# Performance work log

Hardware: AMD Instinct MI355X
Metric: run time of the kernel (lower is better)

Reference implementation:

```python
import jax, jax.numpy as jnp
import numpy as np
import math

B, S, D, H = 4, 2048, 1024, 16
HD = D // H  # head_size = 64


def setup_inputs() -> dict:
    key = jax.random.key(0)
    ks = jax.random.split(key, 12)
    s = 1.0 / math.sqrt(D)
    inp = {
        "query_in": jax.random.normal(ks[0], (B, S, D), jnp.float32),
        "key_in": jax.random.normal(ks[1], (B, S, D), jnp.float32),
        "values_in": jax.random.normal(ks[2], (B, S, D), jnp.float32),
        # causal mask, broadcast over batch and heads
        "mask": jnp.tril(jnp.ones((S, S), jnp.int32))[None, None],
        "Wq": jax.random.normal(ks[3], (D, D), jnp.float32) * s,
        "bq": jnp.zeros((D,), jnp.float32),
        "Wk": jax.random.normal(ks[4], (D, D), jnp.float32) * s,
        "bk": jnp.zeros((D,), jnp.float32),
        "Wv": jax.random.normal(ks[5], (D, D), jnp.float32) * s,
        "bv": jnp.zeros((D,), jnp.float32),
        "Wo": jax.random.normal(ks[6], (D, D), jnp.float32) * s,
        "bo": jnp.zeros((D,), jnp.float32),
    }
    return inp


def _heads(x):
    # [B,S,D] -> [B,H,S,HD]
    return x.reshape(B, S, H, HD).transpose(0, 2, 1, 3)


def reference(query_in, key_in, values_in, mask, Wq, bq, Wk, bk, Wv, bv, Wo, bo):
    q = _heads(query_in @ Wq.T + bq)
    k = _heads(key_in @ Wk.T + bk)
    v = _heads(values_in @ Wv.T + bv)
    # scaled dot-product scores [B,H,Sq,Sk]
    att = jnp.einsum("bhqd,bhkd->bhqk", q, k) / math.sqrt(HD)
    att = jnp.where(mask == 0, jnp.float32(-1e9), att)
    # NOTE: original module applies dropout (identity at eval / p=0) directly
    # to scores with NO softmax -- faithfully reproduced here.
    out = jnp.einsum("bhqk,bhkd->bhqd", att, v)
    out = out.transpose(0, 2, 1, 3).reshape(B, S, D)
    return out @ Wo.T + bo
```

## Files before the change

### kernel.cpp

```cpp
#include <hip/hip_runtime.h>
#include <stdint.h>

typedef unsigned short ushort_t;
typedef __bf16 bf16x8 __attribute__((ext_vector_type(8)));
typedef float f32x4 __attribute__((ext_vector_type(4)));
typedef ushort_t us4 __attribute__((ext_vector_type(4)));

#define MFMA16(a, b, c) __builtin_amdgcn_mfma_f32_16x16x32_bf16((a), (b), (c), 0, 0, 0)

constexpr int Bn = 4, Sn = 2048, Dn = 1024, Hn = 16, HDn = 64;
constexpr float SCALE = 0.125f;
constexpr float NEG = -1e9f;

__device__ __forceinline__ float bf2f(ushort_t u) {
  unsigned x = ((unsigned)u) << 16;
  return __builtin_bit_cast(float, x);
}
__device__ __forceinline__ ushort_t f2bf(float f) {
  unsigned x = __builtin_bit_cast(unsigned, f);
  x = x + 0x7FFFu + ((x >> 16) & 1u);
  return (ushort_t)(x >> 16);
}
__device__ __forceinline__ uint4 ld8_f32_bf16(const float* __restrict__ p) {
  float4 a = *(const float4*)p;
  float4 b = *(const float4*)(p + 4);
  union { ushort_t u[8]; uint4 v; } r;
  r.u[0] = f2bf(a.x); r.u[1] = f2bf(a.y); r.u[2] = f2bf(a.z); r.u[3] = f2bf(a.w);
  r.u[4] = f2bf(b.x); r.u[5] = f2bf(b.y); r.u[6] = f2bf(b.z); r.u[7] = f2bf(b.w);
  return r.v;
}
__device__ __forceinline__ void gl2lds16(const void* g, void* l) {
  __builtin_amdgcn_global_load_lds(
      (__attribute__((address_space(1))) void*)g,
      (__attribute__((address_space(3))) void*)l, 16, 0, 0);
}

__global__ __launch_bounds__(256)
void cvt_all(const float* __restrict__ xq, const float* __restrict__ xk,
             const float* __restrict__ xv, const float* __restrict__ wq,
             const float* __restrict__ wk, const float* __restrict__ wv,
             const float* __restrict__ wo, ushort_t* __restrict__ Xd,
             ushort_t* __restrict__ Wd) {
  const int bid = blockIdx.x;
  if (bid < 12288) {
    const int which = bid >> 12;
    const float* s = which == 0 ? xq : which == 1 ? xk : xv;
    size_t i = ((size_t)(bid & 4095) * 256 + threadIdx.x) * 8;
    *(uint4*)(Xd + (size_t)which * 8388608 + i) = ld8_f32_bf16(s + i);
  } else {
    const int wb = bid - 12288, which = wb >> 9;
    const float* s = which == 0 ? wq : which == 1 ? wk : which == 2 ? wv : wo;
    size_t i = ((size_t)(wb & 511) * 256 + threadIdx.x) * 8;
    *(uint4*)(Wd + (size_t)which * 1048576 + i) = ld8_f32_bf16(s + i);
  }
}

__global__ __launch_bounds__(256, 4)
void gemm_qkv(const ushort_t* __restrict__ Xb, const ushort_t* __restrict__ Wb,
              const float* __restrict__ bq, const float* __restrict__ bk,
              const float* __restrict__ bv, ushort_t* __restrict__ Qd,
              ushort_t* __restrict__ Ktd, ushort_t* __restrict__ Vtd,
              float* __restrict__ Rs) {
  constexpr int K = 1024;
  __shared__ __align__(16) ushort_t As[128 * 64];
  __shared__ __align__(16) ushort_t Bs[128 * 64];

  const int z = blockIdx.z;
  const ushort_t* A  = Xb + (size_t)z * 8388608;
  const ushort_t* Wt = Wb + (size_t)z * 1048576;
  const float* bias = z == 0 ? bq : z == 1 ? bk : bv;
  ushort_t* Cp = z == 0 ? Qd : z == 1 ? Ktd : Vtd;

  const int tid = threadIdx.x;
  const int lane = tid & 63, w = tid >> 6;
  const int quad = lane >> 4, l16 = lane & 15;
  const int wm = w >> 1, wn = w & 1;
  const int row0 = blockIdx.x * 128;
  const int col0 = blockIdx.y * 128;

  const int sr = lane >> 3;
  const int sg = ((lane & 7) ^ (sr & 7)) * 8;
  const ushort_t* Ab = A  + (size_t)(row0 + w * 32 + sr) * K + sg;
  const ushort_t* Bb = Wt + (size_t)(col0 + w * 32 + sr) * K + sg;

  f32x4 acc[4][4] = {};

  for (int k0 = 0; k0 < K; k0 += 64) {
    __syncthreads();
#pragma unroll
    for (int i = 0; i < 4; ++i) {
      gl2lds16(Ab + (size_t)(i * 8) * K + k0, &As[(w * 32 + i * 8) * 64]);
      gl2lds16(Bb + (size_t)(i * 8) * K + k0, &Bs[(w * 32 + i * 8) * 64]);
    }
    __syncthreads();
#pragma unroll
    for (int ks = 0; ks < 2; ++ks) {
      const int kg = ((ks * 4 + quad) ^ (l16 & 7)) * 8;
      bf16x8 af[4], bfr[4];
#pragma unroll
      for (int mt = 0; mt < 4; ++mt)
        af[mt] = *(const bf16x8*)(&As[(wm * 64 + mt * 16 + l16) * 64 + kg]);
#pragma unroll
      for (int nt = 0; nt < 4; ++nt)
        bfr[nt] = *(const bf16x8*)(&Bs[(wn * 64 + nt * 16 + l16) * 64 + kg]);
#pragma unroll
      for (int mt = 0; mt < 4; ++mt)
#pragma unroll
        for (int nt = 0; nt < 4; ++nt)
          acc[mt][nt] = MFMA16(af[mt], bfr[nt], acc[mt][nt]);
    }
  }

#pragma unroll
  for (int mt = 0; mt < 4; ++mt) {
#pragma unroll
    for (int nt = 0; nt < 4; ++nt) {
      const int col = col0 + wn * 64 + nt * 16 + l16;
      const float bv4 = bias[col];
      const int rowb = row0 + wm * 64 + mt * 16 + quad * 4;
      if (z != 0) {
        const int b = rowb >> 11, s = rowb & (Sn - 1);
        const int h = col >> 6, hd = col & 63;
        us4 pk;
#pragma unroll
        for (int r = 0; r < 4; ++r) pk[r] = f2bf(acc[mt][nt][r] + bv4);
        *(us4*)(Cp + ((size_t)((b * Hn + h) * HDn + hd)) * Sn + s) = pk;
      } else {
#pragma unroll
        for (int r = 0; r < 4; ++r) {
          const int row = rowb + r;
          const int b = row >> 11, s = row & (Sn - 1);
          const int h = col >> 6, hd = col & 63;
          Cp[(((size_t)(b * Hn + h) * Sn + s) << 6) + hd] = f2bf(acc[mt][nt][r] + bv4);
        }
      }
    }
  }

  if (z == 2) {
    const int b = row0 >> 11;
    const int t = ((row0 & (Sn - 1)) >> 6) + wm;
#pragma unroll
    for (int nt = 0; nt < 4; ++nt) {
      const int col = col0 + wn * 64 + nt * 16 + l16;
      const float bv4 = bias[col];
      float p = 0.f;
#pragma unroll
      for (int mt = 0; mt < 4; ++mt)
#pragma unroll
        for (int r = 0; r < 4; ++r) p += acc[mt][nt][r] + bv4;
      p += __shfl_xor(p, 16);
      p += __shfl_xor(p, 32);
      if (quad == 0) {
        const int h = col >> 6, n = col & 63;
        Rs[((size_t)(b * Hn + h) * 32 + t) * 64 + n] = p;
      }
    }
  }
}

__global__ __launch_bounds__(256, 4)
void gemm_out(const ushort_t* __restrict__ A, const ushort_t* __restrict__ Wt,
              const float* __restrict__ bias, float* __restrict__ Cp) {
  constexpr int K = 1024;
  __shared__ __align__(16) ushort_t As[128 * 64];
  __shared__ __align__(16) ushort_t Bs[128 * 64];

  const int tid = threadIdx.x;
  const int lane = tid & 63, w = tid >> 6;
  const int quad = lane >> 4, l16 = lane & 15;
  const int wm = w >> 1, wn = w & 1;
  const int row0 = blockIdx.x * 128;
  const int col0 = blockIdx.y * 128;

  const int sr = lane >> 3;
  const int sg = ((lane & 7) ^ (sr & 7)) * 8;
  const ushort_t* Ab = A  + (size_t)(row0 + w * 32 + sr) * K + sg;
  const ushort_t* Bb = Wt + (size_t)(col0 + w * 32 + sr) * K + sg;

  f32x4 acc[4][4] = {};

  for (int k0 = 0; k0 < K; k0 += 64) {
    __syncthreads();
#pragma unroll
    for (int i = 0; i < 4; ++i) {
      gl2lds16(Ab + (size_t)(i * 8) * K + k0, &As[(w * 32 + i * 8) * 64]);
      gl2lds16(Bb + (size_t)(i * 8) * K + k0, &Bs[(w * 32 + i * 8) * 64]);
    }
    __syncthreads();
#pragma unroll
    for (int ks = 0; ks < 2; ++ks) {
      const int kg = ((ks * 4 + quad) ^ (l16 & 7)) * 8;
      bf16x8 af[4], bfr[4];
#pragma unroll
      for (int mt = 0; mt < 4; ++mt)
        af[mt] = *(const bf16x8*)(&As[(wm * 64 + mt * 16 + l16) * 64 + kg]);
#pragma unroll
      for (int nt = 0; nt < 4; ++nt)
        bfr[nt] = *(const bf16x8*)(&Bs[(wn * 64 + nt * 16 + l16) * 64 + kg]);
#pragma unroll
      for (int mt = 0; mt < 4; ++mt)
#pragma unroll
        for (int nt = 0; nt < 4; ++nt)
          acc[mt][nt] = MFMA16(af[mt], bfr[nt], acc[mt][nt]);
    }
  }

#pragma unroll
  for (int mt = 0; mt < 4; ++mt)
#pragma unroll
    for (int nt = 0; nt < 4; ++nt) {
      const int col = col0 + wn * 64 + nt * 16 + l16;
      const float bv = bias[col];
      const int rowb = row0 + wm * 64 + mt * 16 + quad * 4;
#pragma unroll
      for (int r = 0; r < 4; ++r)
        Cp[(size_t)(rowb + r) * 1024 + col] = acc[mt][nt][r] + bv;
    }
}

__global__ __launch_bounds__(256)
void scan_attn2(const ushort_t* __restrict__ Q, const ushort_t* __restrict__ Kt,
                const ushort_t* __restrict__ Vt, const float* __restrict__ Rs,
                ushort_t* __restrict__ O) {
  __shared__ __align__(16) ushort_t Kp[2][4096];
  __shared__ __align__(16) ushort_t Vts[2][4096];
  __shared__ __align__(16) ushort_t Zs[4096];
  __shared__ __align__(16) ushort_t Ks[4096];
  __shared__ __align__(16) ushort_t Ss[64][72];
  __shared__ __align__(16) float sfx[4][64];

  const int tid = threadIdx.x, lane = tid & 63, w = tid >> 6;
  const int quad = lane >> 4, l16 = lane & 15;
  const int bh = blockIdx.x;
  const int g = blockIdx.y;
  const int qt0 = g * 4;
  const int b = bh >> 4, h = bh & 15;
  const ushort_t* Qb  = Q  + (size_t)bh * Sn * HDn;
  const ushort_t* Ktb = Kt + (size_t)bh * HDn * Sn;
  const ushort_t* Vtb = Vt + (size_t)bh * HDn * Sn;
  const float* Rb = Rs + (size_t)bh * 32 * 64;

  const int sr = lane >> 3;
  const int sg = ((lane & 7) ^ (sr & 7)) * 8;
  const int q8 = lane & 7, h8 = lane >> 3;

  f32x4 pzacc[4] = {};
  if (qt0 > 0) {
#pragma unroll
    for (int c = 0; c < 2; ++c) {
      const int row = w * 16 + c * 8;
      gl2lds16(Ktb + (size_t)(row + sr) * Sn + sg, &Kp[0][row * 64]);
      gl2lds16(Vtb + (size_t)(row + sr) * Sn + sg, &Vts[0][row * 64]);
    }
    for (int tau = 0; tau < qt0; ++tau) {
      const int pc = tau & 1;
      __syncthreads();
      if (tau + 1 < qt0) {
#pragma unroll
        for (int c = 0; c < 2; ++c) {
          const int row = w * 16 + c * 8;
          gl2lds16(Ktb + (size_t)(row + sr) * Sn + (tau + 1) * 64 + sg, &Kp[1 - pc][row * 64]);
          gl2lds16(Vtb + (size_t)(row + sr) * Sn + (tau + 1) * 64 + sg, &Vts[1 - pc][row * 64]);
        }
      }
#pragma unroll
      for (int ks = 0; ks < 2; ++ks) {
        const int kg = ((ks * 4 + quad) ^ (l16 & 7)) * 8;
        bf16x8 ak = *(const bf16x8*)(&Kp[pc][(w * 16 + l16) * 64 + kg]);
#pragma unroll
        for (int nt = 0; nt < 4; ++nt) {
          bf16x8 bv8 = *(const bf16x8*)(&Vts[pc][(nt * 16 + l16) * 64 + kg]);
          pzacc[nt] = MFMA16(ak, bv8, pzacc[nt]);
        }
      }
    }
    __syncthreads();
  }

  uint4  kvr[2][2];
  bf16x8 bqr[2][2];
  {
    const int q0 = qt0 * 64;
#pragma unroll
    for (int c = 0; c < 2; ++c) {
      const int row = w * 16 + c * 8;
      gl2lds16(Vtb + (size_t)(row + sr) * Sn + q0 + sg, &Vts[0][row * 64]);
      kvr[0][c] = *(const uint4*)(Ktb + (size_t)(w * 16 + c * 8 + h8) * Sn + q0 + q8 * 8);
    }
#pragma unroll
    for (int ks = 0; ks < 2; ++ks)
      bqr[0][ks] = *(const bf16x8*)(Qb + (size_t)(q0 + w * 16 + l16) * HDn + (ks * 4 + quad) * 8);
  }

  if (tid < 64) {
    float acc = 0.f;
    for (int tau = 31; tau >= qt0; --tau) {
      if (tau < qt0 + 4) sfx[tau - qt0][tid] = acc;
      acc += Rb[(size_t)tau * 64 + tid];
    }
  }

#pragma unroll 4
  for (int i = 0; i < 4; ++i) {
    const int cur = i & 1;
    const int qt = qt0 + i, q0 = qt * 64;

    __syncthreads();

#pragma unroll
    for (int nt = 0; nt < 4; ++nt) {
      const int n = nt * 16 + l16;
      const int d0 = w * 16 + quad * 4;
      us4 pk;
#pragma unroll
      for (int r = 0; r < 4; ++r) pk[r] = f2bf(SCALE * pzacc[nt][r]);
      *(us4*)(&Zs[n * 64 + (((d0 >> 3) ^ (n & 7)) << 3) + (d0 & 7)]) = pk;
    }
#pragma unroll
    for (int c = 0; c < 2; ++c) {
      const int hd = w * 16 + c * 8 + h8;
      const int G = hd >> 3;
      const ushort_t* ku = (const ushort_t*)&kvr[cur][c];
#pragma unroll
      for (int j = 0; j < 8; ++j) {
        const int e = (j + q8) & 7;
        const int s = q8 * 8 + e;
        Ks[s * 64 + ((G ^ e) << 3) + (hd & 7)] = ku[e];
      }
    }
#pragma unroll
    for (int c = 0; c < 2; ++c) {
      const int hd = w * 16 + c * 8 + h8;
      *(uint4*)(&Kp[0][hd * 64 + ((q8 ^ (hd & 7)) << 3)]) = kvr[cur][c];
    }

    __syncthreads();

    if (i < 3) {
      const int q1 = (qt + 1) * 64, nxt = 1 - cur;
#pragma unroll
      for (int c = 0; c < 2; ++c) {
        const int row = w * 16 + c * 8;
        gl2lds16(Vtb + (size_t)(row + sr) * Sn + q1 + sg, &Vts[nxt][row * 64]);
        kvr[nxt][c] = *(const uint4*)(Ktb + (size_t)(w * 16 + c * 8 + h8) * Sn + q1 + q8 * 8);
      }
#pragma unroll
      for (int ks = 0; ks < 2; ++ks)
        bqr[nxt][ks] = *(const bf16x8*)(Qb + (size_t)(q1 + w * 16 + l16) * HDn + (ks * 4 + quad) * 8);
    }

    f32x4 oacc[4] = {};
#pragma unroll
    for (int ks = 0; ks < 2; ++ks) {
      const int kg = ((ks * 4 + quad) ^ (l16 & 7)) * 8;
#pragma unroll
      for (int nt = 0; nt < 4; ++nt) {
        bf16x8 az = *(const bf16x8*)(&Zs[(nt * 16 + l16) * 64 + kg]);
        oacc[nt] = MFMA16(az, bqr[cur][ks], oacc[nt]);
      }
    }
    f32x4 sacc[4] = {};
#pragma unroll
    for (int ks = 0; ks < 2; ++ks) {
      const int kg = ((ks * 4 + quad) ^ (l16 & 7)) * 8;
#pragma unroll
      for (int nt = 0; nt < 4; ++nt) {
        bf16x8 ak = *(const bf16x8*)(&Ks[(nt * 16 + l16) * 64 + kg]);
        sacc[nt] = MFMA16(ak, bqr[cur][ks], sacc[nt]);
      }
    }
    const int qrel = w * 16 + l16;
#pragma unroll
    for (int nt = 0; nt < 4; ++nt) {
      const int kb = nt * 16 + quad * 4;
      us4 pk;
#pragma unroll
      for (int r = 0; r < 4; ++r) {
        float val = (kb + r > qrel) ? NEG : sacc[nt][r] * SCALE;
        pk[r] = f2bf(val);
      }
      *(us4*)(&Ss[qrel][kb]) = pk;
    }
#pragma unroll
    for (int ks = 0; ks < 2; ++ks) {
      bf16x8 bs = *(const bf16x8*)(&Ss[qrel][ks * 32 + quad * 8]);
#pragma unroll
      for (int nt = 0; nt < 4; ++nt) {
        bf16x8 av = *(const bf16x8*)(&Vts[cur][(nt * 16 + l16) * 64 + (((ks * 4 + quad) ^ (l16 & 7)) << 3)]);
        oacc[nt] = MFMA16(av, bs, oacc[nt]);
      }
    }

    const int s = q0 + w * 16 + l16;
#pragma unroll
    for (int nt = 0; nt < 4; ++nt) {
      const int nb = nt * 16 + quad * 4;
      float4 s4 = *(const float4*)(&sfx[i][nb]);
      us4 pk;
      pk[0] = f2bf(oacc[nt][0] + NEG * s4.x);
      pk[1] = f2bf(oacc[nt][1] + NEG * s4.y);
      pk[2] = f2bf(oacc[nt][2] + NEG * s4.z);
      pk[3] = f2bf(oacc[nt][3] + NEG * s4.w);
      *(us4*)(&O[((size_t)(b * Sn + s)) * Dn + h * 64 + nb]) = pk;
    }

    if (i < 3) {
#pragma unroll
      for (int ks = 0; ks < 2; ++ks) {
        const int kg = ((ks * 4 + quad) ^ (l16 & 7)) * 8;
        bf16x8 ak = *(const bf16x8*)(&Kp[0][(w * 16 + l16) * 64 + kg]);
#pragma unroll
        for (int nt = 0; nt < 4; ++nt) {
          bf16x8 bv8 = *(const bf16x8*)(&Vts[cur][(nt * 16 + l16) * 64 + kg]);
          pzacc[nt] = MFMA16(ak, bv8, pzacc[nt]);
        }
      }
    }
  }
}

extern "C" void kernel_launch(void* const* d_in, const int* in_sizes, int n_in,
                              void* d_out, int out_size, void* d_ws, size_t ws_size,
                              hipStream_t stream) {
  const float* Xq = (const float*)d_in[0];
  const float* Xk = (const float*)d_in[1];
  const float* Xv = (const float*)d_in[2];
  const float* Wq = (const float*)d_in[4];
  const float* bq = (const float*)d_in[5];
  const float* Wk = (const float*)d_in[6];
  const float* bk = (const float*)d_in[7];
  const float* Wv = (const float*)d_in[8];
  const float* bv = (const float*)d_in[9];
  const float* Wo = (const float*)d_in[10];
  const float* bo = (const float*)d_in[11];

  constexpr size_t MiB = 1024 * 1024;
  char* ws = (char*)d_ws;
  ushort_t* Xb  = (ushort_t*)(ws);
  ushort_t* Wb  = (ushort_t*)(ws + 48 * MiB);
  ushort_t* Qb  = (ushort_t*)(ws + 56 * MiB);
  ushort_t* Ktb = (ushort_t*)(ws + 72 * MiB);
  ushort_t* Vtb = (ushort_t*)(ws + 88 * MiB);
  ushort_t* Ob  = (ushort_t*)(ws + 120 * MiB);
  float*    Rsum= (float*)   (ws + 176 * MiB);

  cvt_all<<<14336, 256, 0, stream>>>(Xq, Xk, Xv, Wq, Wk, Wv, Wo, Xb, Wb);
  gemm_qkv<<<dim3(64, 8, 3), 256, 0, stream>>>(Xb, Wb, bq, bk, bv, Qb, Ktb,
                                               Vtb, Rsum);
  scan_attn2<<<dim3(64, 8), 256, 0, stream>>>(Qb, Ktb, Vtb, Rsum, Ob);
  gemm_out<<<dim3(64, 8), 256, 0, stream>>>(Ob, Wb + (size_t)3 * 1048576, bo,
                                            (float*)d_out);
}
```

Before: 290.7 us.

## Split QKV GEMM into three launches, grid-stride conversion, pack attention LDS

The conversion kernel becomes a grid-stride loop over 2048 blocks instead of one block per chunk. The single z-batched QKV GEMM launch is split into three separate launches that take their operands as arguments plus a mode flag. The attention kernel's shared arrays are packed into one 51200-byte buffer in a different order. Together these change how work is spread across the GPU and lower per-block overhead in conversion, at the cost of two extra kernel launches and less concurrency between the three projections.

```diff
diff --git a/kernel.cpp b/kernel.cpp
--- a/kernel.cpp
+++ b/kernel.cpp
@@ -41,35 +41,30 @@
              const float* __restrict__ wk, const float* __restrict__ wv,
              const float* __restrict__ wo, ushort_t* __restrict__ Xd,
              ushort_t* __restrict__ Wd) {
-  const int bid = blockIdx.x;
-  if (bid < 12288) {
-    const int which = bid >> 12;
-    const float* s = which == 0 ? xq : which == 1 ? xk : xv;
-    size_t i = ((size_t)(bid & 4095) * 256 + threadIdx.x) * 8;
-    *(uint4*)(Xd + (size_t)which * 8388608 + i) = ld8_f32_bf16(s + i);
-  } else {
-    const int wb = bid - 12288, which = wb >> 9;
-    const float* s = which == 0 ? wq : which == 1 ? wk : which == 2 ? wv : wo;
-    size_t i = ((size_t)(wb & 511) * 256 + threadIdx.x) * 8;
-    *(uint4*)(Wd + (size_t)which * 1048576 + i) = ld8_f32_bf16(s + i);
+  const unsigned stride = gridDim.x * 256;
+  for (unsigned c = blockIdx.x * 256 + threadIdx.x; c < 3670016u; c += stride) {
+    if (c < 3145728u) {
+      const unsigned which = c >> 20;
+      const float* s = which == 0 ? xq : which == 1 ? xk : xv;
+      size_t i = (size_t)(c & 1048575u) * 8;
+      *(uint4*)(Xd + (size_t)which * 8388608 + i) = ld8_f32_bf16(s + i);
+    } else {
+      const unsigned wc = c - 3145728u;
+      const unsigned which = wc >> 17;
+      const float* s = which == 0 ? wq : which == 1 ? wk : which == 2 ? wv : wo;
+      size_t i = (size_t)(wc & 131071u) * 8;
+      *(uint4*)(Wd + (size_t)which * 1048576 + i) = ld8_f32_bf16(s + i);
+    }
   }
 }
 
 __global__ __launch_bounds__(256, 4)
-void gemm_qkv(const ushort_t* __restrict__ Xb, const ushort_t* __restrict__ Wb,
-              const float* __restrict__ bq, const float* __restrict__ bk,
-              const float* __restrict__ bv, ushort_t* __restrict__ Qd,
-              ushort_t* __restrict__ Ktd, ushort_t* __restrict__ Vtd,
-              float* __restrict__ Rs) {
+void gemm_proj(const ushort_t* __restrict__ A, const ushort_t* __restrict__ Wt,
+               const float* __restrict__ bias, ushort_t* __restrict__ Cp,
+               float* __restrict__ Rs, const int mode) {
   constexpr int K = 1024;
   __shared__ __align__(16) ushort_t As[128 * 64];
   __shared__ __align__(16) ushort_t Bs[128 * 64];
-
-  const int z = blockIdx.z;
-  const ushort_t* A  = Xb + (size_t)z * 8388608;
-  const ushort_t* Wt = Wb + (size_t)z * 1048576;
-  const float* bias = z == 0 ? bq : z == 1 ? bk : bv;
-  ushort_t* Cp = z == 0 ? Qd : z == 1 ? Ktd : Vtd;
 
   const int tid = threadIdx.x;
   const int lane = tid & 63, w = tid >> 6;
@@ -118,7 +113,7 @@
       const int col = col0 + wn * 64 + nt * 16 + l16;
       const float bv4 = bias[col];
       const int rowb = row0 + wm * 64 + mt * 16 + quad * 4;
-      if (z != 0) {
+      if (mode != 0) {
         const int b = rowb >> 11, s = rowb & (Sn - 1);
         const int h = col >> 6, hd = col & 63;
         us4 pk;
@@ -137,7 +132,7 @@
     }
   }
 
-  if (z == 2) {
+  if (mode == 2) {
     const int b = row0 >> 11;
     const int t = ((row0 & (Sn - 1)) >> 6) + wm;
 #pragma unroll
@@ -223,12 +218,13 @@
 void scan_attn2(const ushort_t* __restrict__ Q, const ushort_t* __restrict__ Kt,
                 const ushort_t* __restrict__ Vt, const float* __restrict__ Rs,
                 ushort_t* __restrict__ O) {
-  __shared__ __align__(16) ushort_t Kp[2][4096];
-  __shared__ __align__(16) ushort_t Vts[2][4096];
-  __shared__ __align__(16) ushort_t Zs[4096];
-  __shared__ __align__(16) ushort_t Ks[4096];
-  __shared__ __align__(16) ushort_t Ss[64][72];
-  __shared__ __align__(16) float sfx[4][64];
+  __shared__ __align__(16) char smem[51200];
+  ushort_t* KpB  = (ushort_t*)smem;
+  ushort_t* Zs   = (ushort_t*)(smem + 8192);
+  ushort_t* VtsB = (ushort_t*)(smem + 16384);
+  ushort_t* Ks   = (ushort_t*)(smem + 32768);
+  ushort_t (*Ss)[72] = (ushort_t(*)[72])(smem + 40960);
+  float (*sfx)[64] = (float(*)[64])(smem + 50176);
 
   const int tid = threadIdx.x, lane = tid & 63, w = tid >> 6;
   const int quad = lane >> 4, l16 = lane & 15;
@@ -250,8 +246,8 @@
 #pragma unroll
     for (int c = 0; c < 2; ++c) {
       const int row = w * 16 + c * 8;
-      gl2lds16(Ktb + (size_t)(row + sr) * Sn + sg, &Kp[0][row * 64]);
-      gl2lds16(Vtb + (size_t)(row + sr) * Sn + sg, &Vts[0][row * 64]);
+      gl2lds16(Ktb + (size_t)(row + sr) * Sn + sg, &KpB[row * 64]);
+      gl2lds16(Vtb + (size_t)(row + sr) * Sn + sg, &VtsB[row * 64]);
     }
     for (int tau = 0; tau < qt0; ++tau) {
       const int pc = tau & 1;
@@ -260,17 +256,19 @@
 #pragma unroll
         for (int c = 0; c < 2; ++c) {
           const int row = w * 16 + c * 8;
-          gl2lds16(Ktb + (size_t)(row + sr) * Sn + (tau + 1) * 64 + sg, &Kp[1 - pc][row * 64]);
-          gl2lds16(Vtb + (size_t)(row + sr) * Sn + (tau + 1) * 64 + sg, &Vts[1 - pc][row * 64]);
+          gl2lds16(Ktb + (size_t)(row + sr) * Sn + (tau + 1) * 64 + sg,
+                   &KpB[(1 - pc) * 4096 + row * 64]);
+          gl2lds16(Vtb + (size_t)(row + sr) * Sn + (tau + 1) * 64 + sg,
+                   &VtsB[(1 - pc) * 4096 + row * 64]);
         }
       }
 #pragma unroll
       for (int ks = 0; ks < 2; ++ks) {
         const int kg = ((ks * 4 + quad) ^ (l16 & 7)) * 8;
-        bf16x8 ak = *(const bf16x8*)(&Kp[pc][(w * 16 + l16) * 64 + kg]);
+        bf16x8 ak = *(const bf16x8*)(&KpB[pc * 4096 + (w * 16 + l16) * 64 + kg]);
 #pragma unroll
         for (int nt = 0; nt < 4; ++nt) {
-          bf16x8 bv8 = *(const bf16x8*)(&Vts[pc][(nt * 16 + l16) * 64 + kg]);
+          bf16x8 bv8 = *(const bf16x8*)(&VtsB[pc * 4096 + (nt * 16 + l16) * 64 + kg]);
           pzacc[nt] = MFMA16(ak, bv8, pzacc[nt]);
         }
       }
@@ -285,7 +283,7 @@
 #pragma unroll
     for (int c = 0; c < 2; ++c) {
       const int row = w * 16 + c * 8;
-      gl2lds16(Vtb + (size_t)(row + sr) * Sn + q0 + sg, &Vts[0][row * 64]);
+      gl2lds16(Vtb + (size_t)(row + sr) * Sn + q0 + sg, &VtsB[row * 64]);
       kvr[0][c] = *(const uint4*)(Ktb + (size_t)(w * 16 + c * 8 + h8) * Sn + q0 + q8 * 8);
     }
 #pragma unroll
@@ -332,7 +330,7 @@
 #pragma unroll
     for (int c = 0; c < 2; ++c) {
       const int hd = w * 16 + c * 8 + h8;
-      *(uint4*)(&Kp[0][hd * 64 + ((q8 ^ (hd & 7)) << 3)]) = kvr[cur][c];
+      *(uint4*)(&KpB[hd * 64 + ((q8 ^ (hd & 7)) << 3)]) = kvr[cur][c];
     }
 
     __syncthreads();
@@ -342,7 +340,7 @@
 #pragma unroll
       for (int c = 0; c < 2; ++c) {
         const int row = w * 16 + c * 8;
-        gl2lds16(Vtb + (size_t)(row + sr) * Sn + q1 + sg, &Vts[nxt][row * 64]);
+        gl2lds16(Vtb + (size_t)(row + sr) * Sn + q1 + sg, &VtsB[nxt * 4096 + row * 64]);
         kvr[nxt][c] = *(const uint4*)(Ktb + (size_t)(w * 16 + c * 8 + h8) * Sn + q1 + q8 * 8);
       }
 #pragma unroll
@@ -387,7 +385,7 @@
       bf16x8 bs = *(const bf16x8*)(&Ss[qrel][ks * 32 + quad * 8]);
 #pragma unroll
       for (int nt = 0; nt < 4; ++nt) {
-        bf16x8 av = *(const bf16x8*)(&Vts[cur][(nt * 16 + l16) * 64 + (((ks * 4 + quad) ^ (l16 & 7)) << 3)]);
+        bf16x8 av = *(const bf16x8*)(&VtsB[cur * 4096 + (nt * 16 + l16) * 64 + (((ks * 4 + quad) ^ (l16 & 7)) << 3)]);
         oacc[nt] = MFMA16(av, bs, oacc[nt]);
       }
     }
@@ -409,10 +407,10 @@
 #pragma unroll
       for (int ks = 0; ks < 2; ++ks) {
         const int kg = ((ks * 4 + quad) ^ (l16 & 7)) * 8;
-        bf16x8 ak = *(const bf16x8*)(&Kp[0][(w * 16 + l16) * 64 + kg]);
+        bf16x8 ak = *(const bf16x8*)(&KpB[(w * 16 + l16) * 64 + kg]);
 #pragma unroll
         for (int nt = 0; nt < 4; ++nt) {
-          bf16x8 bv8 = *(const bf16x8*)(&Vts[cur][(nt * 16 + l16) * 64 + kg]);
+          bf16x8 bv8 = *(const bf16x8*)(&VtsB[cur * 4096 + (nt * 16 + l16) * 64 + kg]);
           pzacc[nt] = MFMA16(ak, bv8, pzacc[nt]);
         }
       }
@@ -445,9 +443,14 @@
   ushort_t* Ob  = (ushort_t*)(ws + 120 * MiB);
   float*    Rsum= (float*)   (ws + 176 * MiB);
 
-  cvt_all<<<14336, 256, 0, stream>>>(Xq, Xk, Xv, Wq, Wk, Wv, Wo, Xb, Wb);
-  gemm_qkv<<<dim3(64, 8, 3), 256, 0, stream>>>(Xb, Wb, bq, bk, bv, Qb, Ktb,
-                                               Vtb, Rsum);
+  cvt_all<<<2048, 256, 0, stream>>>(Xq, Xk, Xv, Wq, Wk, Wv, Wo, Xb, Wb);
+  gemm_proj<<<dim3(64, 8), 256, 0, stream>>>(Xb, Wb, bq, Qb, Rsum, 0);
+  gemm_proj<<<dim3(64, 8), 256, 0, stream>>>(Xb + (size_t)1 * 8388608,
+                                             Wb + (size_t)1 * 1048576, bk, Ktb,
+                                             Rsum, 1);
+  gemm_proj<<<dim3(64, 8), 256, 0, stream>>>(Xb + (size_t)2 * 8388608,
+                                             Wb + (size_t)2 * 1048576, bv, Vtb,
+                                             Rsum, 2);
   scan_attn2<<<dim3(64, 8), 256, 0, stream>>>(Qb, Ktb, Vtb, Rsum, Ob);
   gemm_out<<<dim3(64, 8), 256, 0, stream>>>(Ob, Wb + (size_t)3 * 1048576, bo,
                                             (float*)d_out);
```

Measured after the change: 306.9 us. +5.6%, slower.
